# Kernel tuning notes

Measured on AMD Instinct MI355X. Metric: run time of the kernel, lower is better.

The kernel has to match this reference:

```python
import jax, jax.numpy as jnp
import numpy as np

N, E, B = 24000, 96000, 1200
NPG = N // B  # nodes per graph

def _lin(k, fi, fo):
    s = 1.0 / np.sqrt(fi)
    return jax.random.uniform(k, (fi, fo), jnp.float32, -s, s)

def setup_inputs():
    key = jax.random.key(0)
    ks = jax.random.split(key, 32)
    x = jax.random.normal(ks[0], (N, 9), jnp.float32)
    edge_attr = jax.random.normal(ks[1], (E, 4), jnp.float32)
    src = jax.random.randint(ks[2], (E,), 0, N)
    # destination node within the same graph as the source (block-diagonal adjacency)
    dst = (src // NPG) * NPG + jax.random.randint(ks[3], (E,), 0, NPG)
    edge_index = jnp.stack([src, dst]).astype(jnp.int32)
    batch = (jnp.arange(N) // NPG).astype(jnp.int32)
    fp_batch = jax.random.normal(ks[4], (B, 2048), jnp.float32)
    p = dict(
        Wq1=_lin(ks[5], 9, 512), bq1=jnp.zeros(512, jnp.float32),
        Wk1=_lin(ks[6], 9, 512), bk1=jnp.zeros(512, jnp.float32),
        Wv1=_lin(ks[7], 9, 512), bv1=jnp.zeros(512, jnp.float32),
        We1=_lin(ks[8], 4, 512),
        Ws1=_lin(ks[9], 9, 512), bs1=jnp.zeros(512, jnp.float32),
        Wq2=_lin(ks[10], 512, 1024), bq2=jnp.zeros(1024, jnp.float32),
        Wk2=_lin(ks[11], 512, 1024), bk2=jnp.zeros(1024, jnp.float32),
        Wv2=_lin(ks[12], 512, 1024), bv2=jnp.zeros(1024, jnp.float32),
        We2=_lin(ks[13], 4, 1024),
        Ws2=_lin(ks[14], 512, 1024), bs2=jnp.zeros(1024, jnp.float32),
        Wfp=_lin(ks[15], 2048, 256), bfp=jnp.zeros(256, jnp.float32),
        Wfin=_lin(ks[16], 1280, 1024), bfin=jnp.zeros(1024, jnp.float32),
    )
    return dict(x=x, edge_index=edge_index, edge_attr=edge_attr, batch=batch, fp_batch=fp_batch, **p)

def _tconv(x, src, dst, ea, Wq, bq, Wk, bk, Wv, bv, We, Ws, bs, H, C):
    """PyG TransformerConv: concat=True, beta=False, root_weight=True."""
    n = x.shape[0]
    q = (x @ Wq + bq).reshape(n, H, C)
    k = (x @ Wk + bk).reshape(n, H, C)
    v = (x @ Wv + bv).reshape(n, H, C)
    e = (ea @ We).reshape(-1, H, C)            # lin_edge has no bias
    ke = k[src] + e                            # [E,H,C]
    alpha = jnp.einsum('ehc,ehc->eh', q[dst], ke) / jnp.sqrt(jnp.float32(C))
    # scatter-softmax over incoming edges of each target node
    amax = jax.ops.segment_max(alpha, dst, num_segments=n)
    amax = jnp.where(jnp.isfinite(amax), amax, 0.0)  # nodes with no in-edges
    ex = jnp.exp(alpha - amax[dst])
    den = jax.ops.segment_sum(ex, dst, num_segments=n)[dst] + 1e-16
    msg = (v[src] + e) * (ex / den)[:, :, None]
    out = jax.ops.segment_sum(msg, dst, num_segments=n).reshape(n, H * C)
    return out + x @ Ws + bs                   # root/skip connection

def reference(x, edge_index, edge_attr, batch, fp_batch, Wq1, bq1, Wk1, bk1, Wv1, bv1, We1, Ws1, bs1, Wq2, bq2, Wk2, bk2, Wv2, bv2, We2, Ws2, bs2, Wfp, bfp, Wfin, bfin):
    src, dst = edge_index[0], edge_index[1]
    h = jax.nn.relu(_tconv(x, src, dst, edge_attr, Wq1, bq1, Wk1, bk1, Wv1, bv1, We1, Ws1, bs1, 4, 128))
    h = _tconv(h, src, dst, edge_attr, Wq2, bq2, Wk2, bk2, Wv2, bv2, We2, Ws2, bs2, 4, 256)
    cnt = jax.ops.segment_sum(jnp.ones((h.shape[0],), h.dtype), batch, num_segments=B)
    g = jax.ops.segment_sum(h, batch, num_segments=B) / cnt[:, None]  # global_mean_pool
    fp = fp_batch @ Wfp + bfp
    return jnp.concatenate([g, fp], axis=-1) @ Wfin + bfin
```

## Files before the change

### kernel.cpp

```cpp
#include <hip/hip_runtime.h>
#include <cstdint>
#include <cstddef>

static constexpr int NN = 24000;
static constexpr int NE = 96000;
static constexpr int NB = 1200;
static constexpr int NPG = 20;
static constexpr int MPAD = 24064;

typedef __attribute__((ext_vector_type(8))) short bfv8;
typedef __attribute__((ext_vector_type(4))) float fv4;

__device__ __forceinline__ unsigned f2ord(float f){
  unsigned u = __float_as_uint(f);
  return (u & 0x80000000u) ? ~u : (u | 0x80000000u);
}
__device__ __forceinline__ float ord2f(unsigned u){
  return (u & 0x80000000u) ? __uint_as_float(u & 0x7FFFFFFFu)
                           : __uint_as_float(~u);
}
__device__ __forceinline__ unsigned short f2bf(float f){
  unsigned u = __float_as_uint(f);
  u += 0x7FFFu + ((u >> 16) & 1u);
  return (unsigned short)(u >> 16);
}
__device__ __forceinline__ float bf2f(unsigned short s){
  return __uint_as_float(((unsigned)s) << 16);
}

__global__ __launch_bounds__(256) void count_kernel(const int* __restrict__ dst,
                                                    unsigned* __restrict__ deg)
{
  int e = blockIdx.x*256 + threadIdx.x;
  if (e < NE) atomicAdd(&deg[dst[e]], 1u);
}

__global__ __launch_bounds__(1024) void scan_kernel(const unsigned* __restrict__ deg,
                                                    unsigned* __restrict__ rowstart)
{
  __shared__ unsigned s[1024];
  __shared__ unsigned carry_s;
  int tid = threadIdx.x;
  if (tid == 0) carry_s = 0;
  __syncthreads();
  for (int base = 0; base < NN; base += 1024){
    unsigned v = (base + tid < NN) ? deg[base + tid] : 0u;
    s[tid] = v;
    __syncthreads();
#pragma unroll
    for (int off = 1; off < 1024; off <<= 1){
      unsigned t = (tid >= off) ? s[tid - off] : 0u;
      __syncthreads();
      s[tid] += t;
      __syncthreads();
    }
    unsigned carry = carry_s;
    if (base + tid < NN) rowstart[base + tid] = carry + s[tid] - v;
    __syncthreads();
    if (tid == 0) carry_s = carry + s[1023];
    __syncthreads();
  }
  if (tid == 0) rowstart[NN] = carry_s;
}

__global__ __launch_bounds__(256) void scatter_kernel(const int* __restrict__ dst,
                                                      const unsigned* __restrict__ rowstart,
                                                      unsigned* __restrict__ cur,
                                                      int* __restrict__ eidx)
{
  int e = blockIdx.x*256 + threadIdx.x;
  if (e >= NE) return;
  int d = dst[e];
  unsigned p = rowstart[d] + atomicAdd(&cur[d], 1u);
  eidx[p] = e;
}

template<bool BA, bool BB>
__global__ __launch_bounds__(256) void node_gemm_l1_pair(
    const float* __restrict__ x,
    const float* __restrict__ Wa, const float* __restrict__ ba,
    const float* __restrict__ Wb, const float* __restrict__ bb,
    void* __restrict__ outa, void* __restrict__ outb)
{
  int t = blockIdx.x*256 + threadIdx.x;
  if (t >= NN*512) return;
  int n = t >> 9, j = t & 511;
  float xr[9];
#pragma unroll
  for (int i=0;i<9;i++) xr[i] = x[n*9+i];
  float aa=ba[j], ab=bb[j];
#pragma unroll
  for (int i=0;i<9;i++){
    float xi = xr[i];
    aa += xi*Wa[i*512+j];
    ab += xi*Wb[i*512+j];
  }
  if (BA) ((unsigned short*)outa)[t] = f2bf(aa); else ((float*)outa)[t] = aa;
  if (BB) ((unsigned short*)outb)[t] = f2bf(ab); else ((float*)outb)[t] = ab;
}

__global__ __launch_bounds__(256) void alpha_bf16_hc512(
    const unsigned short* __restrict__ q, const unsigned short* __restrict__ k,
    const float* __restrict__ ea, const float* __restrict__ We,
    const int* __restrict__ src, const int* __restrict__ dst,
    float* __restrict__ alpha, unsigned* __restrict__ amax)
{
  int wave = (blockIdx.x*256 + threadIdx.x) >> 6;
  int lane = threadIdx.x & 63;
  if (wave >= NE) return;
  int e = wave;
  int s = src[e], d = dst[e];
  float ea0=ea[e*4+0], ea1=ea[e*4+1], ea2=ea[e*4+2], ea3=ea[e*4+3];
  const float scale = 0.088388347648318447f;
  int off = lane*8;
  bfv8 qv = *reinterpret_cast<const bfv8*>(q + (size_t)d*512 + off);
  bfv8 kv = *reinterpret_cast<const bfv8*>(k + (size_t)s*512 + off);
  float part = 0.f;
#pragma unroll
  for (int j=0;j<8;j++){
    int f = off + j;
    float ef = ea0*We[f] + ea1*We[512+f] + ea2*We[1024+f] + ea3*We[1536+f];
    part += bf2f((unsigned short)qv[j]) * (bf2f((unsigned short)kv[j]) + ef);
  }
#pragma unroll
  for (int o=8; o>=1; o>>=1) part += __shfl_xor(part, o);
  if ((lane & 15) == 0){
    int h = lane >> 4;
    float a = part*scale;
    alpha[e*4+h] = a;
    atomicMax(&amax[d*4+h], f2ord(a));
  }
}

__global__ __launch_bounds__(256) void alpha_bf16_hc1024(
    const unsigned short* __restrict__ q, const unsigned short* __restrict__ k,
    const float* __restrict__ ea, const float* __restrict__ We,
    const int* __restrict__ src, const int* __restrict__ dst,
    float* __restrict__ alpha, unsigned* __restrict__ amax)
{
  int wave = (blockIdx.x*256 + threadIdx.x) >> 6;
  int lane = threadIdx.x & 63;
  if (wave >= NE) return;
  int e = wave;
  int s = src[e], d = dst[e];
  float ea0=ea[e*4+0], ea1=ea[e*4+1], ea2=ea[e*4+2], ea3=ea[e*4+3];
  const float scale = 1.0f/16.0f;
#pragma unroll
  for (int p=0;p<2;p++){
    int off = p*512 + lane*8;
    bfv8 qv = *reinterpret_cast<const bfv8*>(q + (size_t)d*1024 + off);
    bfv8 kv = *reinterpret_cast<const bfv8*>(k + (size_t)s*1024 + off);
    float part = 0.f;
#pragma unroll
    for (int j=0;j<8;j++){
      int f = off + j;
      float ef = ea0*We[f] + ea1*We[1024+f] + ea2*We[2048+f] + ea3*We[3072+f];
      part += bf2f((unsigned short)qv[j]) * (bf2f((unsigned short)kv[j]) + ef);
    }
#pragma unroll
    for (int o=16; o>=1; o>>=1) part += __shfl_xor(part, o);
    if ((lane & 31) == 0){
      int h = p*2 + (lane>>5);
      float a = part*scale;
      alpha[e*4+h] = a;
      atomicMax(&amax[d*4+h], f2ord(a));
    }
  }
}

__global__ __launch_bounds__(256) void ex_kernel(
    float* __restrict__ alpha, const unsigned* __restrict__ amax,
    const int* __restrict__ dst, float* __restrict__ den)
{
  int t = blockIdx.x*256 + threadIdx.x;
  if (t >= NE*4) return;
  int e = t>>2, h = t&3;
  int d = dst[e];
  float m = ord2f(amax[d*4+h]);
  float v = __expf(alpha[t]-m);
  alpha[t] = v;
  unsafeAtomicAdd(&den[d*4+h], v);
}

__global__ __launch_bounds__(256) void gather512_kernel(
    const unsigned short* __restrict__ v, const float* __restrict__ ea,
    const float* __restrict__ We,
    const int* __restrict__ src,
    const unsigned* __restrict__ rowstart, const int* __restrict__ eidx,
    const float* __restrict__ exw, const float* __restrict__ den,
    const float* __restrict__ accin, unsigned short* __restrict__ hb)
{
  int n = blockIdx.x;
  int tid = threadIdx.x;
  int h = tid >> 6;
  int f2 = tid*2;
  unsigned p0 = rowstart[n], p1 = rowstart[n+1];
  float2 W0 = *reinterpret_cast<const float2*>(We + 0*512 + f2);
  float2 W1 = *reinterpret_cast<const float2*>(We + 1*512 + f2);
  float2 W2 = *reinterpret_cast<const float2*>(We + 2*512 + f2);
  float2 W3 = *reinterpret_cast<const float2*>(We + 3*512 + f2);
  float rdn = 1.0f / (den[n*4+h] + 1e-16f);
  float2 s = *reinterpret_cast<const float2*>(accin + (size_t)n*512 + f2);
  for (unsigned p = p0; p < p1; ++p){
    int e  = eidx[p];
    float w = exw[e*4+h] * rdn;
    float4 eav = *reinterpret_cast<const float4*>(ea + (size_t)e*4);
    ushort2 vv = *reinterpret_cast<const ushort2*>(v + (size_t)src[e]*512 + f2);
    float efx = eav.x*W0.x + eav.y*W1.x + eav.z*W2.x + eav.w*W3.x;
    float efy = eav.x*W0.y + eav.y*W1.y + eav.z*W2.y + eav.w*W3.y;
    s.x += w*(bf2f(vv.x) + efx);
    s.y += w*(bf2f(vv.y) + efy);
  }
  ushort2 o;
  o.x = f2bf(fmaxf(s.x, 0.0f));
  o.y = f2bf(fmaxf(s.y, 0.0f));
  *reinterpret_cast<ushort2*>(hb + (size_t)n*512 + f2) = o;
}

__global__ __launch_bounds__(256) void gather1024_kernel(
    const unsigned short* __restrict__ v, const float* __restrict__ ea,
    const float* __restrict__ We,
    const int* __restrict__ src,
    const unsigned* __restrict__ rowstart, const int* __restrict__ eidx,
    const float* __restrict__ exw, const float* __restrict__ den,
    float* __restrict__ acc)
{
  int n = blockIdx.x;
  int tid = threadIdx.x;
  int h = tid >> 6;
  int f4 = tid*4;
  unsigned p0 = rowstart[n], p1 = rowstart[n+1];
  float4 W0 = *reinterpret_cast<const float4*>(We + 0*1024 + f4);
  float4 W1 = *reinterpret_cast<const float4*>(We + 1*1024 + f4);
  float4 W2 = *reinterpret_cast<const float4*>(We + 2*1024 + f4);
  float4 W3 = *reinterpret_cast<const float4*>(We + 3*1024 + f4);
  float rdn = 1.0f / (den[n*4+h] + 1e-16f);
  float4 s = *reinterpret_cast<float4*>(acc + (size_t)n*1024 + f4);
  for (unsigned p = p0; p < p1; ++p){
    int e  = eidx[p];
    float w = exw[e*4+h] * rdn;
    float4 eav = *reinterpret_cast<const float4*>(ea + (size_t)e*4);
    ushort4 vv = *reinterpret_cast<const ushort4*>(v + (size_t)src[e]*1024 + f4);
    s.x += w*(bf2f(vv.x) + eav.x*W0.x + eav.y*W1.x + eav.z*W2.x + eav.w*W3.x);
    s.y += w*(bf2f(vv.y) + eav.x*W0.y + eav.y*W1.y + eav.z*W2.y + eav.w*W3.y);
    s.z += w*(bf2f(vv.z) + eav.x*W0.z + eav.y*W1.z + eav.z*W2.z + eav.w*W3.z);
    s.w += w*(bf2f(vv.w) + eav.x*W0.w + eav.y*W1.w + eav.z*W2.w + eav.w*W3.w);
  }
  *reinterpret_cast<float4*>(acc + (size_t)n*1024 + f4) = s;
}

__global__ __launch_bounds__(256) void cvt_wt_kernel(const float* __restrict__ W,
                                                     unsigned short* __restrict__ Wt)
{
  int t = blockIdx.x*256 + threadIdx.x;
  if (t >= 1024*512) return;
  int n = t >> 9, k = t & 511;
  Wt[t] = f2bf(W[k*1024 + n]);
}

template<bool BOUT>
__global__ __launch_bounds__(256) void gemm_bf16_mfma(
    const unsigned short* __restrict__ A,
    const unsigned short* __restrict__ B,
    const float* __restrict__ bias,
    void* __restrict__ Cout, int M)
{
  constexpr int K = 512, N = 1024;
  __shared__ unsigned short As[128*32];
  __shared__ unsigned short Bs[128*32];
  int tid  = threadIdx.x;
  int wid  = tid >> 6, lane = tid & 63;
  int wr   = wid >> 1, wc = wid & 1;
  int bm   = blockIdx.y * 128, bn = blockIdx.x * 128;
  int l15  = lane & 15, kg = lane >> 4;

  int r0 = (wid*2+0)*16 + (lane>>2);
  int r1 = (wid*2+1)*16 + (lane>>2);
  int s0 = lane & 3;
  int kc0 = s0 ^ ((r0>>1)&3);
  int kc1 = s0 ^ ((r1>>1)&3);
  unsigned short* ldsA0 = As + (wid*2+0)*512;
  unsigned short* ldsA1 = As + (wid*2+1)*512;
  unsigned short* ldsB0 = Bs + (wid*2+0)*512;
  unsigned short* ldsB1 = Bs + (wid*2+1)*512;

  fv4 acc[4][4];
#pragma unroll
  for (int m=0;m<4;m++)
#pragma unroll
    for (int n=0;n<4;n++) acc[m][n] = (fv4){0.f,0.f,0.f,0.f};

  for (int k0 = 0; k0 < K; k0 += 32){
    __syncthreads();
    __builtin_amdgcn_global_load_lds(
        (const __attribute__((address_space(1))) void*)(A + (size_t)(bm+r0)*K + k0 + kc0*8),
        (__attribute__((address_space(3))) void*)ldsA0, 16, 0, 0);
    __builtin_amdgcn_global_load_lds(
        (const __attribute__((address_space(1))) void*)(A + (size_t)(bm+r1)*K + k0 + kc1*8),
        (__attribute__((address_space(3))) void*)ldsA1, 16, 0, 0);
    __builtin_amdgcn_global_load_lds(
        (const __attribute__((address_space(1))) void*)(B + (size_t)(bn+r0)*K + k0 + kc0*8),
        (__attribute__((address_space(3))) void*)ldsB0, 16, 0, 0);
    __builtin_amdgcn_global_load_lds(
        (const __attribute__((address_space(1))) void*)(B + (size_t)(bn+r1)*K + k0 + kc1*8),
        (__attribute__((address_space(3))) void*)ldsB1, 16, 0, 0);
    __syncthreads();
    bfv8 af[4], bfr[4];
#pragma unroll
    for (int m=0;m<4;m++){
      int r  = wr*64 + m*16 + l15;
      int sl = kg ^ ((r>>1)&3);
      af[m] = *reinterpret_cast<const bfv8*>(reinterpret_cast<char*>(As) + r*64 + sl*16);
    }
#pragma unroll
    for (int n=0;n<4;n++){
      int r  = wc*64 + n*16 + l15;
      int sl = kg ^ ((r>>1)&3);
      bfr[n] = *reinterpret_cast<const bfv8*>(reinterpret_cast<char*>(Bs) + r*64 + sl*16);
    }
#pragma unroll
    for (int m=0;m<4;m++)
#pragma unroll
      for (int n=0;n<4;n++)
        acc[m][n] = __builtin_amdgcn_mfma_f32_16x16x32_bf16(af[m], bfr[n], acc[m][n], 0, 0, 0);
  }
#pragma unroll
  for (int m=0;m<4;m++){
#pragma unroll
    for (int n=0;n<4;n++){
      int col = bn + wc*64 + n*16 + l15;
      float bcol = bias[col];
#pragma unroll
      for (int r=0;r<4;r++){
        int row = bm + wr*64 + m*16 + (lane>>4)*4 + r;
        if (row < M){
          float val = acc[m][n][r] + bcol;
          if (BOUT) ((unsigned short*)Cout)[(size_t)row*N + col] = f2bf(val);
          else      ((float*)Cout)[(size_t)row*N + col] = val;
        }
      }
    }
  }
}

__global__ __launch_bounds__(256) void sgemm_partial(
    const float* __restrict__ A, const float* __restrict__ W,
    float* __restrict__ P, int M, int N, int K, int kchunk, int zoff)
{
  __shared__ float As[32][68];
  __shared__ __align__(16) float Bs[32][64];
  int tid = threadIdx.x;
  int bm = blockIdx.y*64, bn = blockIdx.x*64;
  int kbeg = blockIdx.z*kchunk;
  int kend = min(kbeg + kchunk, K);
  float* Pz = P + (size_t)(zoff + blockIdx.z)*M*N;
  int ty = tid >> 4, tx = tid & 15;
  float acc[4][4] = {};
  for (int k0 = kbeg; k0 < kend; k0 += 32){
#pragma unroll
    for (int i=0;i<2;i++){
      int lin = tid + i*256;
      int r = lin >> 3;
      int kq = (lin & 7) * 4;
      float4 av = make_float4(0.f,0.f,0.f,0.f);
      int row = bm + r;
      if (row < M) av = *reinterpret_cast<const float4*>(A + (size_t)row*K + k0 + kq);
      As[kq+0][r]=av.x; As[kq+1][r]=av.y; As[kq+2][r]=av.z; As[kq+3][r]=av.w;
    }
#pragma unroll
    for (int i=0;i<2;i++){
      int lin = tid + i*256;
      int kr = lin >> 4;
      int c4 = (lin & 15) * 4;
      float4 wv = *reinterpret_cast<const float4*>(W + (size_t)(k0+kr)*N + bn + c4);
      *reinterpret_cast<float4*>(&Bs[kr][c4]) = wv;
    }
    __syncthreads();
#pragma unroll
    for (int kk=0;kk<32;kk++){
      float a[4], b[4];
#pragma unroll
      for (int i=0;i<4;i++) a[i] = As[kk][ty*4+i];
#pragma unroll
      for (int j=0;j<4;j++) b[j] = Bs[kk][tx*4+j];
#pragma unroll
      for (int i=0;i<4;i++)
#pragma unroll
        for (int j=0;j<4;j++) acc[i][j] += a[i]*b[j];
    }
    __syncthreads();
  }
#pragma unroll
  for (int i=0;i<4;i++){
    int row = bm + ty*4 + i;
    if (row >= M) break;
#pragma unroll
    for (int j=0;j<4;j++)
      Pz[(size_t)row*N + bn + tx*4 + j] = acc[i][j];
  }
}

__global__ __launch_bounds__(256) void reduce_add_kernel(
    const float* __restrict__ P, const float* __restrict__ bias,
    float* __restrict__ O, int total, int nz, int nmask)
{
  int t = blockIdx.x*256 + threadIdx.x;
  if (t >= total) return;
  float s = bias[t & nmask];
  for (int z = 0; z < nz; ++z) s += P[(size_t)z*total + t];
  O[t] = s;
}

__global__ __launch_bounds__(256) void pool_kernel(const float* __restrict__ h2,
                                                   float* __restrict__ g)
{
  int t = blockIdx.x*256 + threadIdx.x;
  if (t >= NB*256) return;
  int b = t >> 8, f4 = (t & 255) * 4;
  float4 s = make_float4(0.f,0.f,0.f,0.f);
#pragma unroll
  for (int i=0;i<NPG;i++){
    float4 v = *reinterpret_cast<const float4*>(h2 + (size_t)(b*NPG+i)*1024 + f4);
    s.x += v.x; s.y += v.y; s.z += v.z; s.w += v.w;
  }
  s.x *= (1.0f/NPG); s.y *= (1.0f/NPG); s.z *= (1.0f/NPG); s.w *= (1.0f/NPG);
  *reinterpret_cast<float4*>(g + (size_t)b*1024 + f4) = s;
}

extern "C" void kernel_launch(void* const* d_in, const int* in_sizes, int n_in,
                              void* d_out, int out_size, void* d_ws, size_t ws_size,
                              hipStream_t stream)
{
  const float* x    = (const float*)d_in[0];
  const int*   ei   = (const int*)d_in[1];
  const float* ea   = (const float*)d_in[2];
  const float* fpb  = (const float*)d_in[4];
  const float* Wq1  = (const float*)d_in[5];  const float* bq1 = (const float*)d_in[6];
  const float* Wk1  = (const float*)d_in[7];  const float* bk1 = (const float*)d_in[8];
  const float* Wv1  = (const float*)d_in[9];  const float* bv1 = (const float*)d_in[10];
  const float* We1  = (const float*)d_in[11];
  const float* Ws1  = (const float*)d_in[12]; const float* bs1 = (const float*)d_in[13];
  const float* Wq2  = (const float*)d_in[14]; const float* bq2 = (const float*)d_in[15];
  const float* Wk2  = (const float*)d_in[16]; const float* bk2 = (const float*)d_in[17];
  const float* Wv2  = (const float*)d_in[18]; const float* bv2 = (const float*)d_in[19];
  const float* We2  = (const float*)d_in[20];
  const float* Ws2  = (const float*)d_in[21]; const float* bs2 = (const float*)d_in[22];
  const float* Wfp  = (const float*)d_in[23]; const float* bfp = (const float*)d_in[24];
  const float* Wfin = (const float*)d_in[25]; const float* bfin= (const float*)d_in[26];
  const int* src = ei;
  const int* dst = ei + NE;
  float* out = (float*)d_out;

  const size_t F512  = (size_t)NN*512;
  const size_t F1024 = (size_t)NN*1024;
  float* base = (float*)d_ws;
  float* C_a = base;
  float* C_b = base + F1024;
  float* H   = base + 2*F1024;
  unsigned short* q1b = (unsigned short*)C_a;
  unsigned short* v1b = (unsigned short*)C_a;
  unsigned short* k1b = (unsigned short*)H;
  float*          s1  = H;
  unsigned short* hb  = (unsigned short*)C_a + F1024;
  unsigned short* q2b = (unsigned short*)C_a;
  unsigned short* k2b = (unsigned short*)C_b;
  unsigned short* v2b = (unsigned short*)C_a;
  float*          s2  = C_b;
  unsigned short* WtQ = (unsigned short*)H;
  unsigned short* WtK = WtQ + (size_t)1024*512;
  unsigned short* WtV = WtK + (size_t)1024*512;
  unsigned short* WtS = WtV + (size_t)1024*512;
  float* P1 = C_a;
  float* P2 = C_a + 5*(size_t)NB*1024;

  float* tail = base + 2*F1024 + F512;
  float*    alphab   = tail;
  unsigned* amax     = (unsigned*)(alphab + (size_t)NE*4);
  float*    den      = (float*)(amax + (size_t)NN*4);
  unsigned* deg      = (unsigned*)(den + (size_t)NN*4);
  unsigned* cur      = deg + NN;
  unsigned* rowstart = cur + NN;
  int*      eidx     = (int*)(rowstart + NN + 1);
  float*    g        = (float*)(eidx + NE);
  float*    fp       = g + (size_t)NB*1024;

  hipMemsetAsync(deg, 0, sizeof(unsigned)*NN, stream);
  hipMemsetAsync(cur, 0, sizeof(unsigned)*NN, stream);
  count_kernel<<<(NE+255)/256, 256, 0, stream>>>(dst, deg);
  scan_kernel<<<1, 1024, 0, stream>>>(deg, rowstart);
  scatter_kernel<<<(NE+255)/256, 256, 0, stream>>>(dst, rowstart, cur, eidx);

  hipMemsetAsync(amax, 0, sizeof(unsigned)*(size_t)NN*4, stream);
  hipMemsetAsync(den,  0, sizeof(float)*(size_t)NN*4, stream);

  node_gemm_l1_pair<true,true><<<(NN*512+255)/256, 256, 0, stream>>>(
      x, Wq1,bq1, Wk1,bk1, q1b, k1b);
  alpha_bf16_hc512<<<NE/4, 256, 0, stream>>>(q1b, k1b, ea, We1, src, dst, alphab, amax);
  ex_kernel<<<(NE*4+255)/256, 256, 0, stream>>>(alphab, amax, dst, den);
  node_gemm_l1_pair<true,false><<<(NN*512+255)/256, 256, 0, stream>>>(
      x, Wv1,bv1, Ws1,bs1, v1b, s1);
  gather512_kernel<<<NN, 256, 0, stream>>>(v1b, ea, We1, src, rowstart, eidx,
                                           alphab, den, s1, hb);
  hipMemsetAsync(hb + F512, 0, (size_t)(MPAD-NN)*512*sizeof(unsigned short), stream);

  cvt_wt_kernel<<<(1024*512+255)/256, 256, 0, stream>>>(Wq2, WtQ);
  cvt_wt_kernel<<<(1024*512+255)/256, 256, 0, stream>>>(Wk2, WtK);
  cvt_wt_kernel<<<(1024*512+255)/256, 256, 0, stream>>>(Wv2, WtV);
  cvt_wt_kernel<<<(1024*512+255)/256, 256, 0, stream>>>(Ws2, WtS);

  hipMemsetAsync(amax, 0, sizeof(unsigned)*(size_t)NN*4, stream);
  hipMemsetAsync(den,  0, sizeof(float)*(size_t)NN*4, stream);

  {
    dim3 grid(8, MPAD/128);
    gemm_bf16_mfma<true><<<grid, 256, 0, stream>>>(hb, WtQ, bq2, q2b, NN);
    gemm_bf16_mfma<true><<<grid, 256, 0, stream>>>(hb, WtK, bk2, k2b, NN);
  }
  alpha_bf16_hc1024<<<NE/4, 256, 0, stream>>>(q2b, k2b, ea, We2, src, dst, alphab, amax);
  ex_kernel<<<(NE*4+255)/256, 256, 0, stream>>>(alphab, amax, dst, den);
  {
    dim3 grid(8, MPAD/128);
    gemm_bf16_mfma<true><<<grid, 256, 0, stream>>>(hb, WtV, bv2, v2b, NN);
    gemm_bf16_mfma<false><<<grid, 256, 0, stream>>>(hb, WtS, bs2, s2, NN);
  }
  gather1024_kernel<<<NN, 256, 0, stream>>>(v2b, ea, We2, src, rowstart, eidx,
                                            alphab, den, s2);

  pool_kernel<<<(NB*256+255)/256, 256, 0, stream>>>(s2, g);

  {
    dim3 gfp(256/64, (NB+63)/64, 8);
    sgemm_partial<<<gfp, 256, 0, stream>>>(fpb, Wfp, P2, NB, 256, 2048, 256, 0);
    reduce_add_kernel<<<(NB*256+255)/256, 256, 0, stream>>>(P2, bfp, fp, NB*256, 8, 255);
  }
  {
    dim3 g1(1024/64, (NB+63)/64, 4);
    sgemm_partial<<<g1, 256, 0, stream>>>(g, Wfin, P1, NB, 1024, 1024, 256, 0);
    dim3 g2(1024/64, (NB+63)/64, 1);
    sgemm_partial<<<g2, 256, 0, stream>>>(fp, Wfin + (size_t)1024*1024, P1, NB, 1024, 256, 256, 4);
    reduce_add_kernel<<<(NB*1024+255)/256, 256, 0, stream>>>(P1, bfin, out, NB*1024, 5, 1023);
  }
}
```

Baseline: 827.8 us.

## Compute attention logits per graph from shared-memory q/k with precomputed edge projection

Replaces the per-edge alpha kernels with per-graph kernels. Each block loads its graph's q and k rows into LDS once, then walks the CSR in-edges of each destination node. The edge-attribute term is rewritten algebraically as ea·(q·We), using a small per-node projection kernel, so We is no longer re-read per feature per edge. The softmax max is now computed per node in registers and written directly, which removes the atomicMax and its memset. This depends on every edge's source lying in the same 20-node graph as its destination.

```diff
diff --git a/kernel.cpp b/kernel.cpp
--- a/kernel.cpp
+++ b/kernel.cpp
@@ -99,72 +99,163 @@
   if (BB) ((unsigned short*)outb)[t] = f2bf(ab); else ((float*)outb)[t] = ab;
 }
 
-__global__ __launch_bounds__(256) void alpha_bf16_hc512(
-    const unsigned short* __restrict__ q, const unsigned short* __restrict__ k,
-    const float* __restrict__ ea, const float* __restrict__ We,
-    const int* __restrict__ src, const int* __restrict__ dst,
-    float* __restrict__ alpha, unsigned* __restrict__ amax)
+__global__ __launch_bounds__(256) void tproj512_kernel(
+    const unsigned short* __restrict__ q, const float* __restrict__ We,
+    float* __restrict__ t)
 {
   int wave = (blockIdx.x*256 + threadIdx.x) >> 6;
   int lane = threadIdx.x & 63;
-  if (wave >= NE) return;
-  int e = wave;
-  int s = src[e], d = dst[e];
-  float ea0=ea[e*4+0], ea1=ea[e*4+1], ea2=ea[e*4+2], ea3=ea[e*4+3];
-  const float scale = 0.088388347648318447f;
+  if (wave >= NN) return;
   int off = lane*8;
-  bfv8 qv = *reinterpret_cast<const bfv8*>(q + (size_t)d*512 + off);
-  bfv8 kv = *reinterpret_cast<const bfv8*>(k + (size_t)s*512 + off);
-  float part = 0.f;
+  bfv8 qv = *reinterpret_cast<const bfv8*>(q + (size_t)wave*512 + off);
+  float p0=0.f,p1=0.f,p2=0.f,p3=0.f;
 #pragma unroll
   for (int j=0;j<8;j++){
+    float qf = bf2f((unsigned short)qv[j]);
     int f = off + j;
-    float ef = ea0*We[f] + ea1*We[512+f] + ea2*We[1024+f] + ea3*We[1536+f];
-    part += bf2f((unsigned short)qv[j]) * (bf2f((unsigned short)kv[j]) + ef);
-  }
-#pragma unroll
-  for (int o=8; o>=1; o>>=1) part += __shfl_xor(part, o);
+    p0 += qf*We[f]; p1 += qf*We[512+f]; p2 += qf*We[1024+f]; p3 += qf*We[1536+f];
+  }
+#pragma unroll
+  for (int o=8;o>=1;o>>=1){
+    p0 += __shfl_xor(p0,o); p1 += __shfl_xor(p1,o);
+    p2 += __shfl_xor(p2,o); p3 += __shfl_xor(p3,o);
+  }
   if ((lane & 15) == 0){
     int h = lane >> 4;
-    float a = part*scale;
-    alpha[e*4+h] = a;
-    atomicMax(&amax[d*4+h], f2ord(a));
-  }
-}
-
-__global__ __launch_bounds__(256) void alpha_bf16_hc1024(
-    const unsigned short* __restrict__ q, const unsigned short* __restrict__ k,
-    const float* __restrict__ ea, const float* __restrict__ We,
-    const int* __restrict__ src, const int* __restrict__ dst,
-    float* __restrict__ alpha, unsigned* __restrict__ amax)
+    *reinterpret_cast<float4*>(t + (size_t)wave*16 + h*4) = make_float4(p0,p1,p2,p3);
+  }
+}
+
+__global__ __launch_bounds__(256) void tproj1024_kernel(
+    const unsigned short* __restrict__ q, const float* __restrict__ We,
+    float* __restrict__ t)
 {
   int wave = (blockIdx.x*256 + threadIdx.x) >> 6;
   int lane = threadIdx.x & 63;
-  if (wave >= NE) return;
-  int e = wave;
-  int s = src[e], d = dst[e];
-  float ea0=ea[e*4+0], ea1=ea[e*4+1], ea2=ea[e*4+2], ea3=ea[e*4+3];
+  if (wave >= NN) return;
+  float p0=0.f,p1=0.f,p2=0.f,p3=0.f;
+#pragma unroll
+  for (int half=0; half<2; ++half){
+    int off = lane*16 + half*8;
+    bfv8 qv = *reinterpret_cast<const bfv8*>(q + (size_t)wave*1024 + off);
+#pragma unroll
+    for (int j=0;j<8;j++){
+      float qf = bf2f((unsigned short)qv[j]);
+      int f = off + j;
+      p0 += qf*We[f]; p1 += qf*We[1024+f]; p2 += qf*We[2048+f]; p3 += qf*We[3072+f];
+    }
+  }
+#pragma unroll
+  for (int o=8;o>=1;o>>=1){
+    p0 += __shfl_xor(p0,o); p1 += __shfl_xor(p1,o);
+    p2 += __shfl_xor(p2,o); p3 += __shfl_xor(p3,o);
+  }
+  if ((lane & 15) == 0){
+    int h = lane >> 4;
+    *reinterpret_cast<float4*>(t + (size_t)wave*16 + h*4) = make_float4(p0,p1,p2,p3);
+  }
+}
+
+__global__ __launch_bounds__(256) void alpha_g512(
+    const unsigned short* __restrict__ q, const unsigned short* __restrict__ k,
+    const float* __restrict__ ea, const float* __restrict__ t,
+    const int* __restrict__ src,
+    const unsigned* __restrict__ rowstart, const int* __restrict__ eidx,
+    float* __restrict__ alpha, unsigned* __restrict__ amax)
+{
+  __shared__ unsigned short qs[NPG*512];
+  __shared__ unsigned short ks[NPG*512];
+  int g = blockIdx.x, base = g*NPG;
+  int tid = threadIdx.x;
+  for (int c = tid; c < NPG*64; c += 256){
+    int i = c >> 6, col = (c & 63)*8;
+    *reinterpret_cast<uint4*>(qs + i*512 + col) =
+        *reinterpret_cast<const uint4*>(q + (size_t)(base+i)*512 + col);
+    *reinterpret_cast<uint4*>(ks + i*512 + col) =
+        *reinterpret_cast<const uint4*>(k + (size_t)(base+i)*512 + col);
+  }
+  __syncthreads();
+  int w = tid >> 6, lane = tid & 63;
+  const float scale = 0.088388347648318447f;
+  bool hl = (lane & 15) == 0;
+  int h = lane >> 4;
+  for (int dl = w; dl < NPG; dl += 4){
+    int d = base + dl;
+    unsigned p0 = rowstart[d], p1 = rowstart[d+1];
+    float mx = -__builtin_inff();
+    float4 tv = make_float4(0,0,0,0);
+    if (hl) tv = *reinterpret_cast<const float4*>(t + (size_t)d*16 + h*4);
+    bfv8 qv = *reinterpret_cast<const bfv8*>(qs + dl*512 + lane*8);
+    for (unsigned pp = p0; pp < p1; ++pp){
+      int e = eidx[pp];
+      int ls = src[e] - base;
+      bfv8 kv = *reinterpret_cast<const bfv8*>(ks + ls*512 + lane*8);
+      float part = 0.f;
+#pragma unroll
+      for (int j=0;j<8;j++)
+        part += bf2f((unsigned short)qv[j]) * bf2f((unsigned short)kv[j]);
+#pragma unroll
+      for (int o=8;o>=1;o>>=1) part += __shfl_xor(part,o);
+      if (hl){
+        float4 eav = *reinterpret_cast<const float4*>(ea + (size_t)e*4);
+        float a = (part + eav.x*tv.x + eav.y*tv.y + eav.z*tv.z + eav.w*tv.w)*scale;
+        alpha[e*4+h] = a;
+        mx = fmaxf(mx, a);
+      }
+    }
+    if (hl) amax[d*4+h] = f2ord(mx);
+  }
+}
+
+__global__ __launch_bounds__(256) void alpha_g1024(
+    const unsigned short* __restrict__ q, const unsigned short* __restrict__ k,
+    const float* __restrict__ ea, const float* __restrict__ t,
+    const int* __restrict__ src,
+    const unsigned* __restrict__ rowstart, const int* __restrict__ eidx,
+    float* __restrict__ alpha, unsigned* __restrict__ amax)
+{
+  __shared__ unsigned short qs[NPG*512];
+  __shared__ unsigned short ks[NPG*512];
+  int g = blockIdx.x, base = g*NPG;
+  int p = blockIdx.y;
+  int tid = threadIdx.x;
+  for (int c = tid; c < NPG*64; c += 256){
+    int i = c >> 6, col = (c & 63)*8;
+    *reinterpret_cast<uint4*>(qs + i*512 + col) =
+        *reinterpret_cast<const uint4*>(q + (size_t)(base+i)*1024 + p*512 + col);
+    *reinterpret_cast<uint4*>(ks + i*512 + col) =
+        *reinterpret_cast<const uint4*>(k + (size_t)(base+i)*1024 + p*512 + col);
+  }
+  __syncthreads();
+  int w = tid >> 6, lane = tid & 63;
   const float scale = 1.0f/16.0f;
-#pragma unroll
-  for (int p=0;p<2;p++){
-    int off = p*512 + lane*8;
-    bfv8 qv = *reinterpret_cast<const bfv8*>(q + (size_t)d*1024 + off);
-    bfv8 kv = *reinterpret_cast<const bfv8*>(k + (size_t)s*1024 + off);
-    float part = 0.f;
-#pragma unroll
-    for (int j=0;j<8;j++){
-      int f = off + j;
-      float ef = ea0*We[f] + ea1*We[1024+f] + ea2*We[2048+f] + ea3*We[3072+f];
-      part += bf2f((unsigned short)qv[j]) * (bf2f((unsigned short)kv[j]) + ef);
-    }
-#pragma unroll
-    for (int o=16; o>=1; o>>=1) part += __shfl_xor(part, o);
-    if ((lane & 31) == 0){
-      int h = p*2 + (lane>>5);
-      float a = part*scale;
-      alpha[e*4+h] = a;
-      atomicMax(&amax[d*4+h], f2ord(a));
-    }
+  bool hl = (lane & 31) == 0;
+  int h = p*2 + (lane >> 5);
+  for (int dl = w; dl < NPG; dl += 4){
+    int d = base + dl;
+    unsigned p0 = rowstart[d], p1 = rowstart[d+1];
+    float mx = -__builtin_inff();
+    float4 tv = make_float4(0,0,0,0);
+    if (hl) tv = *reinterpret_cast<const float4*>(t + (size_t)d*16 + h*4);
+    bfv8 qv = *reinterpret_cast<const bfv8*>(qs + dl*512 + lane*8);
+    for (unsigned pp = p0; pp < p1; ++pp){
+      int e = eidx[pp];
+      int ls = src[e] - base;
+      bfv8 kv = *reinterpret_cast<const bfv8*>(ks + ls*512 + lane*8);
+      float part = 0.f;
+#pragma unroll
+      for (int j=0;j<8;j++)
+        part += bf2f((unsigned short)qv[j]) * bf2f((unsigned short)kv[j]);
+#pragma unroll
+      for (int o=16;o>=1;o>>=1) part += __shfl_xor(part,o);
+      if (hl){
+        float4 eav = *reinterpret_cast<const float4*>(ea + (size_t)e*4);
+        float a = (part + eav.x*tv.x + eav.y*tv.y + eav.z*tv.z + eav.w*tv.w)*scale;
+        alpha[e*4+h] = a;
+        mx = fmaxf(mx, a);
+      }
+    }
+    if (hl) amax[d*4+h] = f2ord(mx);
   }
 }
 
@@ -483,6 +574,7 @@
   int*      eidx     = (int*)(rowstart + NN + 1);
   float*    g        = (float*)(eidx + NE);
   float*    fp       = g + (size_t)NB*1024;
+  float*    tproj    = fp + (size_t)NB*256;
 
   hipMemsetAsync(deg, 0, sizeof(unsigned)*NN, stream);
   hipMemsetAsync(cur, 0, sizeof(unsigned)*NN, stream);
@@ -490,12 +582,13 @@
   scan_kernel<<<1, 1024, 0, stream>>>(deg, rowstart);
   scatter_kernel<<<(NE+255)/256, 256, 0, stream>>>(dst, rowstart, cur, eidx);
 
-  hipMemsetAsync(amax, 0, sizeof(unsigned)*(size_t)NN*4, stream);
-  hipMemsetAsync(den,  0, sizeof(float)*(size_t)NN*4, stream);
+  hipMemsetAsync(den, 0, sizeof(float)*(size_t)NN*4, stream);
 
   node_gemm_l1_pair<true,true><<<(NN*512+255)/256, 256, 0, stream>>>(
       x, Wq1,bq1, Wk1,bk1, q1b, k1b);
-  alpha_bf16_hc512<<<NE/4, 256, 0, stream>>>(q1b, k1b, ea, We1, src, dst, alphab, amax);
+  tproj512_kernel<<<(NN*64+255)/256, 256, 0, stream>>>(q1b, We1, tproj);
+  alpha_g512<<<NB, 256, 0, stream>>>(q1b, k1b, ea, tproj, src, rowstart, eidx,
+                                     alphab, amax);
   ex_kernel<<<(NE*4+255)/256, 256, 0, stream>>>(alphab, amax, dst, den);
   node_gemm_l1_pair<true,false><<<(NN*512+255)/256, 256, 0, stream>>>(
       x, Wv1,bv1, Ws1,bs1, v1b, s1);
@@ -508,15 +601,19 @@
   cvt_wt_kernel<<<(1024*512+255)/256, 256, 0, stream>>>(Wv2, WtV);
   cvt_wt_kernel<<<(1024*512+255)/256, 256, 0, stream>>>(Ws2, WtS);
 
-  hipMemsetAsync(amax, 0, sizeof(unsigned)*(size_t)NN*4, stream);
-  hipMemsetAsync(den,  0, sizeof(float)*(size_t)NN*4, stream);
+  hipMemsetAsync(den, 0, sizeof(float)*(size_t)NN*4, stream);
 
   {
     dim3 grid(8, MPAD/128);
     gemm_bf16_mfma<true><<<grid, 256, 0, stream>>>(hb, WtQ, bq2, q2b, NN);
     gemm_bf16_mfma<true><<<grid, 256, 0, stream>>>(hb, WtK, bk2, k2b, NN);
   }
-  alpha_bf16_hc1024<<<NE/4, 256, 0, stream>>>(q2b, k2b, ea, We2, src, dst, alphab, amax);
+  tproj1024_kernel<<<(NN*64+255)/256, 256, 0, stream>>>(q2b, We2, tproj);
+  {
+    dim3 ga(NB, 2);
+    alpha_g1024<<<ga, 256, 0, stream>>>(q2b, k2b, ea, tproj, src, rowstart, eidx,
+                                        alphab, amax);
+  }
   ex_kernel<<<(NE*4+255)/256, 256, 0, stream>>>(alphab, amax, dst, den);
   {
     dim3 grid(8, MPAD/128);
```

After: 892.1 us. 1.08x slower.
